# Kernel tuning notes

Hardware: AMD Instinct MI355X
Metric: run time of the kernel (lower is better)

Reference implementation:

```python
import jax, jax.numpy as jnp
import numpy as np

B, N = 2048, 16384
K = 256
TEMPERATURE = 1.0


def entmax15(z):
    # alpha=1.5 entmax via exact sort-based threshold (Peters et al. 2019).
    z = z / 2.0
    zs = jnp.flip(jnp.sort(z, axis=-1), axis=-1)          # descending sort [B, N]
    rho = jnp.arange(1, z.shape[-1] + 1, dtype=z.dtype)   # 1..N
    mean = jnp.cumsum(zs, axis=-1) / rho
    mean_sq = jnp.cumsum(zs * zs, axis=-1) / rho
    ss = rho * (mean_sq - mean * mean)
    delta = jnp.clip((1.0 - ss) / rho, 0.0)
    tau = mean - jnp.sqrt(delta)                           # candidate thresholds
    support = jnp.sum(tau <= zs, axis=-1, keepdims=True)   # support size per row
    tau_star = jnp.take_along_axis(tau, support - 1, axis=-1)
    p = jnp.clip(z - tau_star, 0.0) ** 2
    return p


def setup_inputs() -> dict:
    key = jax.random.key(0)
    logits = jax.random.normal(key, (B, N), dtype=jnp.float32)
    return {"logits": logits}


def reference(logits):
    weights = entmax15(logits / TEMPERATURE)
    # top-k mask + renormalize
    _, topk_idx = jax.lax.top_k(weights, K)                # [B, K]
    mask = jnp.zeros_like(weights).at[
        jnp.arange(weights.shape[0])[:, None], topk_idx
    ].set(1.0)
    weights = weights * mask
    weights = weights / (jnp.sum(weights, axis=-1, keepdims=True) + 1e-8)
    num_selected = jnp.sum(weights > 1e-6, axis=-1)
    return weights, num_selected
```

## Files before the change

kernel.cpp:

```cpp
#include <hip/hip_runtime.h>
#include <math.h>

#define BROWS 2048
#define NCOLS 16384
#define NT    1024
#define V4PT  (NCOLS / NT / 4)
#define CAP   512

__global__ __launch_bounds__(NT, 8)
void entmax_fused(const float* __restrict__ in, float* __restrict__ outw,
                  float* __restrict__ outn)
{
    __shared__ float red[4][16];
    __shared__ float redm[16];
    __shared__ float cand[CAP + 4];
    __shared__ float s_zm, s_T, s_tau, s_S;
    __shared__ int   s_cnt, s_nsel;

    const int row  = blockIdx.x;
    const int tid  = threadIdx.x;
    const int lane = tid & 63;
    const int wid  = tid >> 6;
    const float4* rp4 = (const float4*)(in + (size_t)row * NCOLS);
    float4*       wp4 = (float4*)(outw + (size_t)row * NCOLS);

    if (tid == 0) { s_cnt = 0; s_nsel = 0; }

    float4 zr[V4PT];
    float m = -INFINITY;
    #pragma unroll
    for (int it = 0; it < V4PT; ++it) {
        float4 v = rp4[it * NT + tid];
        v.x *= 0.5f; v.y *= 0.5f; v.z *= 0.5f; v.w *= 0.5f;
        zr[it] = v;
        m = fmaxf(m, fmaxf(fmaxf(v.x, v.y), fmaxf(v.z, v.w)));
    }
    #pragma unroll
    for (int off = 1; off < 64; off <<= 1) m = fmaxf(m, __shfl_xor(m, off));
    if (lane == 0) redm[wid] = m;
    __syncthreads();
    if (tid < 64) {
        float v = (lane < 16) ? redm[lane] : -INFINITY;
        #pragma unroll
        for (int off = 1; off < 16; off <<= 1) v = fmaxf(v, __shfl_xor(v, off));
        if (lane == 0) s_zm = v;
    }
    __syncthreads();
    const float zm = s_zm;

    float g0 = 0.f, g1 = 0.f, g2 = 0.f, g3 = 0.f;
    #pragma unroll
    for (int it = 0; it < V4PT; ++it) {
        float4 v = zr[it];
        #pragma unroll
        for (int e = 0; e < 4; ++e) {
            float z = (e == 0) ? v.x : (e == 1) ? v.y : (e == 2) ? v.z : v.w;
            float d3 = z - (zm - 1.0f);
            if (d3 > 0.f) {
                g3 = fmaf(d3, d3, g3);
                float d2 = d3 - 0.25f; if (d2 > 0.f) g2 = fmaf(d2, d2, g2);
                float d1 = d3 - 0.50f; if (d1 > 0.f) g1 = fmaf(d1, d1, g1);
                float d0 = d3 - 0.75f; if (d0 > 0.f) g0 = fmaf(d0, d0, g0);
            }
        }
    }
    #pragma unroll
    for (int off = 1; off < 64; off <<= 1) {
        g0 += __shfl_xor(g0, off); g1 += __shfl_xor(g1, off);
        g2 += __shfl_xor(g2, off); g3 += __shfl_xor(g3, off);
    }
    if (lane == 0) { red[0][wid] = g0; red[1][wid] = g1; red[2][wid] = g2; red[3][wid] = g3; }
    __syncthreads();
    if (tid < 64) {
        int j = lane >> 4, idx = lane & 15;
        float v = red[j][idx];
        #pragma unroll
        for (int off = 1; off < 16; off <<= 1) v += __shfl_xor(v, off);
        float G0 = __shfl(v, 0), G1 = __shfl(v, 16), G2 = __shfl(v, 32), G3 = __shfl(v, 48);
        (void)G3;
        if (lane == 0) {
            float T = zm - 1.0f;
            if      (G0 >= 1.02f) T = zm - 0.25f;
            else if (G1 >= 1.02f) T = zm - 0.50f;
            else if (G2 >= 1.02f) T = zm - 0.75f;
            s_T = T;
        }
    }
    __syncthreads();
    const float T = s_T;

    #pragma unroll
    for (int it = 0; it < V4PT; ++it) {
        float4 v = zr[it];
        if (v.x > T) { int p = atomicAdd(&s_cnt, 1); if (p < CAP) cand[p] = v.x; }
        if (v.y > T) { int p = atomicAdd(&s_cnt, 1); if (p < CAP) cand[p] = v.y; }
        if (v.z > T) { int p = atomicAdd(&s_cnt, 1); if (p < CAP) cand[p] = v.z; }
        if (v.w > T) { int p = atomicAdd(&s_cnt, 1); if (p < CAP) cand[p] = v.w; }
    }
    __syncthreads();

    if (tid < 64) {
        const int C = min(s_cnt, CAP);
        if (lane < 4) cand[C + lane] = -INFINITY;
        const int C4 = (C + 3) >> 2;
        const float4* c4 = (const float4*)cand;
        float lo = T, hi = zm;
        for (int round = 0; round < 3; ++round) {
            float h = (hi - lo) * 0.015625f;
            float t = fmaf(h, (float)(lane + 1), lo);
            float g = 0.f;
            for (int i = 0; i < C4; ++i) {
                float4 v = c4[i]; float d;
                d = v.x - t; if (d > 0.f) g = fmaf(d, d, g);
                d = v.y - t; if (d > 0.f) g = fmaf(d, d, g);
                d = v.z - t; if (d > 0.f) g = fmaf(d, d, g);
                d = v.w - t; if (d > 0.f) g = fmaf(d, d, g);
            }
            unsigned long long bal = __ballot(g >= 1.f);
            float lo_old = lo;
            if (bal == 0ull) hi = lo_old + h;
            else {
                int j = 63 - (int)__clzll((long long)bal);
                lo = fmaf(h, (float)(j + 1), lo_old);
                hi = fmaf(h, (float)(j + 2), lo_old);
            }
        }
        float tau = lo;
        for (int r = 0; r < 3; ++r) {
            float k = 0.f, s1 = 0.f, s2 = 0.f;
            for (int i = 0; i < C4; ++i) {
                float4 v = c4[i];
                if (v.x > tau) { k += 1.f; s1 += v.x; s2 = fmaf(v.x, v.x, s2); }
                if (v.y > tau) { k += 1.f; s1 += v.y; s2 = fmaf(v.y, v.y, s2); }
                if (v.z > tau) { k += 1.f; s1 += v.z; s2 = fmaf(v.z, v.z, s2); }
                if (v.w > tau) { k += 1.f; s1 += v.w; s2 = fmaf(v.w, v.w, s2); }
            }
            if (k < 0.5f) break;
            float mean  = s1 / k;
            float ss    = s2 - mean * s1;
            float delta = fmaxf((1.f - ss) / k, 0.f);
            tau = mean - sqrtf(delta);
        }
        float ps = 0.f;
        for (int i = 0; i < C4; ++i) {
            float4 v = c4[i]; float d;
            d = v.x - tau; if (d > 0.f) ps = fmaf(d, d, ps);
            d = v.y - tau; if (d > 0.f) ps = fmaf(d, d, ps);
            d = v.z - tau; if (d > 0.f) ps = fmaf(d, d, ps);
            d = v.w - tau; if (d > 0.f) ps = fmaf(d, d, ps);
        }
        if (lane == 0) { s_tau = tau; s_S = ps; }
    }
    __syncthreads();
    const float tau_star = s_tau;
    const float rnorm    = 1.0f / (s_S + 1e-8f);

    int lc = 0;
    #pragma unroll
    for (int it = 0; it < V4PT; ++it) {
        float4 v = zr[it];
        float4 w; float d;
        d = fmaxf(v.x - tau_star, 0.f); w.x = d * d * rnorm; lc += (w.x > 1e-6f);
        d = fmaxf(v.y - tau_star, 0.f); w.y = d * d * rnorm; lc += (w.y > 1e-6f);
        d = fmaxf(v.z - tau_star, 0.f); w.z = d * d * rnorm; lc += (w.z > 1e-6f);
        d = fmaxf(v.w - tau_star, 0.f); w.w = d * d * rnorm; lc += (w.w > 1e-6f);
        wp4[it * NT + tid] = w;
    }
    #pragma unroll
    for (int off = 32; off; off >>= 1) lc += __shfl_down(lc, off);
    if (lane == 0) atomicAdd(&s_nsel, lc);
    __syncthreads();
    if (tid == 0) outn[row] = (float)s_nsel;
}

extern "C" void kernel_launch(void* const* d_in, const int* in_sizes, int n_in,
                              void* d_out, int out_size, void* d_ws, size_t ws_size,
                              hipStream_t stream) {
    const float* logits = (const float*)d_in[0];
    float* outw = (float*)d_out;
    float* outn = outw + (size_t)BROWS * NCOLS;
    entmax_fused<<<dim3(BROWS), dim3(NT), 0, stream>>>(logits, outw, outn);
}
```

Measured before the change: 255.0 us.

## Parallelize candidate threshold search across all warps and use nontemporal stores

The single-warp bisection and Newton-style refinement over the candidate buffer is split across all 16 wavefronts. Partial sums go through shared-memory double buffers, and each thread now redundantly reduces the per-warp partials instead of waiting on an extra barrier-and-broadcast step. This is meant to remove the serial tail where 15 of 16 warps sit idle. The candidate cap grows to 1024 so one candidate maps to one thread, and output stores become nontemporal to avoid polluting the cache. The cost is more barriers and redundant reads of the shared-memory reductions.

```diff
diff --git a/kernel.cpp b/kernel.cpp
--- a/kernel.cpp
+++ b/kernel.cpp
@@ -5,24 +5,28 @@
 #define NCOLS 16384
 #define NT    1024
 #define V4PT  (NCOLS / NT / 4)
-#define CAP   512
+#define NW    (NT / 64)
+#define CAP   1024
+
+typedef float vfloat4 __attribute__((ext_vector_type(4)));
 
 __global__ __launch_bounds__(NT, 8)
 void entmax_fused(const float* __restrict__ in, float* __restrict__ outw,
                   float* __restrict__ outn)
 {
-    __shared__ float red[4][16];
-    __shared__ float redm[16];
-    __shared__ float cand[CAP + 4];
-    __shared__ float s_zm, s_T, s_tau, s_S;
-    __shared__ int   s_cnt, s_nsel;
+    __shared__ float  cand[CAP + 4];
+    __shared__ float  redm[NW];
+    __shared__ float  red[4][NW];
+    __shared__ float  gpart[2][NW][64];
+    __shared__ float4 rpart[2][NW];
+    __shared__ int    s_cnt, s_nsel;
 
-    const int row  = blockIdx.x;
     const int tid  = threadIdx.x;
     const int lane = tid & 63;
     const int wid  = tid >> 6;
+    const int row  = blockIdx.x;
     const float4* rp4 = (const float4*)(in + (size_t)row * NCOLS);
-    float4*       wp4 = (float4*)(outw + (size_t)row * NCOLS);
+    vfloat4*      wp4 = (vfloat4*)(outw + (size_t)row * NCOLS);
 
     if (tid == 0) { s_cnt = 0; s_nsel = 0; }
 
@@ -39,14 +43,9 @@
     for (int off = 1; off < 64; off <<= 1) m = fmaxf(m, __shfl_xor(m, off));
     if (lane == 0) redm[wid] = m;
     __syncthreads();
-    if (tid < 64) {
-        float v = (lane < 16) ? redm[lane] : -INFINITY;
-        #pragma unroll
-        for (int off = 1; off < 16; off <<= 1) v = fmaxf(v, __shfl_xor(v, off));
-        if (lane == 0) s_zm = v;
-    }
-    __syncthreads();
-    const float zm = s_zm;
+    float zm = -INFINITY;
+    #pragma unroll
+    for (int w = 0; w < NW; ++w) zm = fmaxf(zm, redm[w]);
 
     float g0 = 0.f, g1 = 0.f, g2 = 0.f, g3 = 0.f;
     #pragma unroll
@@ -71,23 +70,13 @@
     }
     if (lane == 0) { red[0][wid] = g0; red[1][wid] = g1; red[2][wid] = g2; red[3][wid] = g3; }
     __syncthreads();
-    if (tid < 64) {
-        int j = lane >> 4, idx = lane & 15;
-        float v = red[j][idx];
-        #pragma unroll
-        for (int off = 1; off < 16; off <<= 1) v += __shfl_xor(v, off);
-        float G0 = __shfl(v, 0), G1 = __shfl(v, 16), G2 = __shfl(v, 32), G3 = __shfl(v, 48);
-        (void)G3;
-        if (lane == 0) {
-            float T = zm - 1.0f;
-            if      (G0 >= 1.02f) T = zm - 0.25f;
-            else if (G1 >= 1.02f) T = zm - 0.50f;
-            else if (G2 >= 1.02f) T = zm - 0.75f;
-            s_T = T;
-        }
-    }
-    __syncthreads();
-    const float T = s_T;
+    float G0 = 0.f, G1 = 0.f, G2 = 0.f;
+    #pragma unroll
+    for (int w = 0; w < NW; ++w) { G0 += red[0][w]; G1 += red[1][w]; G2 += red[2][w]; }
+    float T = zm - 1.0f;
+    if      (G0 >= 1.02f) T = zm - 0.25f;
+    else if (G1 >= 1.02f) T = zm - 0.50f;
+    else if (G2 >= 1.02f) T = zm - 0.75f;
 
     #pragma unroll
     for (int it = 0; it < V4PT; ++it) {
@@ -98,73 +87,96 @@
         if (v.w > T) { int p = atomicAdd(&s_cnt, 1); if (p < CAP) cand[p] = v.w; }
     }
     __syncthreads();
+    const int C = min(s_cnt, CAP);
+    if (tid < 4) cand[C + tid] = -INFINITY;
+    __syncthreads();
 
-    if (tid < 64) {
-        const int C = min(s_cnt, CAP);
-        if (lane < 4) cand[C + lane] = -INFINITY;
-        const int C4 = (C + 3) >> 2;
-        const float4* c4 = (const float4*)cand;
-        float lo = T, hi = zm;
-        for (int round = 0; round < 3; ++round) {
-            float h = (hi - lo) * 0.015625f;
-            float t = fmaf(h, (float)(lane + 1), lo);
-            float g = 0.f;
-            for (int i = 0; i < C4; ++i) {
-                float4 v = c4[i]; float d;
-                d = v.x - t; if (d > 0.f) g = fmaf(d, d, g);
-                d = v.y - t; if (d > 0.f) g = fmaf(d, d, g);
-                d = v.z - t; if (d > 0.f) g = fmaf(d, d, g);
-                d = v.w - t; if (d > 0.f) g = fmaf(d, d, g);
-            }
-            unsigned long long bal = __ballot(g >= 1.f);
-            float lo_old = lo;
-            if (bal == 0ull) hi = lo_old + h;
-            else {
-                int j = 63 - (int)__clzll((long long)bal);
-                lo = fmaf(h, (float)(j + 1), lo_old);
-                hi = fmaf(h, (float)(j + 2), lo_old);
-            }
+    const int C4    = (C + 3) >> 2;
+    const int chunk = (C4 + NW - 1) / NW;
+    const int i0    = wid * chunk;
+    const int i1    = min(i0 + chunk, C4);
+    const float4* c4 = (const float4*)cand;
+
+    float lo = T, hi = zm;
+    for (int round = 0; round < 3; ++round) {
+        const int buf = round & 1;
+        float h = (hi - lo) * 0.015625f;
+        float t = fmaf(h, (float)(lane + 1), lo);
+        float g = 0.f;
+        for (int i = i0; i < i1; ++i) {
+            float4 v = c4[i]; float d;
+            d = v.x - t; if (d > 0.f) g = fmaf(d, d, g);
+            d = v.y - t; if (d > 0.f) g = fmaf(d, d, g);
+            d = v.z - t; if (d > 0.f) g = fmaf(d, d, g);
+            d = v.w - t; if (d > 0.f) g = fmaf(d, d, g);
         }
-        float tau = lo;
-        for (int r = 0; r < 3; ++r) {
-            float k = 0.f, s1 = 0.f, s2 = 0.f;
-            for (int i = 0; i < C4; ++i) {
-                float4 v = c4[i];
-                if (v.x > tau) { k += 1.f; s1 += v.x; s2 = fmaf(v.x, v.x, s2); }
-                if (v.y > tau) { k += 1.f; s1 += v.y; s2 = fmaf(v.y, v.y, s2); }
-                if (v.z > tau) { k += 1.f; s1 += v.z; s2 = fmaf(v.z, v.z, s2); }
-                if (v.w > tau) { k += 1.f; s1 += v.w; s2 = fmaf(v.w, v.w, s2); }
-            }
-            if (k < 0.5f) break;
+        gpart[buf][wid][lane] = g;
+        __syncthreads();
+        float gs = 0.f;
+        #pragma unroll
+        for (int w = 0; w < NW; ++w) gs += gpart[buf][w][lane];
+        unsigned long long bal = __ballot(gs >= 1.0f);
+        float lo_old = lo;
+        if (bal == 0ull) hi = lo_old + h;
+        else {
+            int j = 63 - (int)__clzll((long long)bal);
+            lo = fmaf(h, (float)(j + 1), lo_old);
+            hi = fmaf(h, (float)(j + 2), lo_old);
+        }
+    }
+
+    float tau = lo;
+    const float cz = (tid < C) ? cand[tid] : -INFINITY;
+    for (int r = 0; r < 3; ++r) {
+        const int buf = r & 1;
+        float k = 0.f, s1 = 0.f, s2 = 0.f;
+        if (cz > tau) { k = 1.f; s1 = cz; s2 = cz * cz; }
+        #pragma unroll
+        for (int off = 1; off < 64; off <<= 1) {
+            k  += __shfl_xor(k,  off);
+            s1 += __shfl_xor(s1, off);
+            s2 += __shfl_xor(s2, off);
+        }
+        if (lane == 0) rpart[buf][wid] = make_float4(k, s1, s2, 0.f);
+        __syncthreads();
+        k = 0.f; s1 = 0.f; s2 = 0.f;
+        #pragma unroll
+        for (int w = 0; w < NW; ++w) {
+            float4 p = rpart[buf][w]; k += p.x; s1 += p.y; s2 += p.z;
+        }
+        if (k >= 0.5f) {
             float mean  = s1 / k;
             float ss    = s2 - mean * s1;
             float delta = fmaxf((1.f - ss) / k, 0.f);
             tau = mean - sqrtf(delta);
         }
+    }
+
+    float rnorm;
+    {
         float ps = 0.f;
-        for (int i = 0; i < C4; ++i) {
-            float4 v = c4[i]; float d;
-            d = v.x - tau; if (d > 0.f) ps = fmaf(d, d, ps);
-            d = v.y - tau; if (d > 0.f) ps = fmaf(d, d, ps);
-            d = v.z - tau; if (d > 0.f) ps = fmaf(d, d, ps);
-            d = v.w - tau; if (d > 0.f) ps = fmaf(d, d, ps);
-        }
-        if (lane == 0) { s_tau = tau; s_S = ps; }
+        float d = cz - tau;
+        if (d > 0.f) ps = d * d;
+        #pragma unroll
+        for (int off = 1; off < 64; off <<= 1) ps += __shfl_xor(ps, off);
+        if (lane == 0) rpart[1][wid] = make_float4(ps, 0.f, 0.f, 0.f);
+        __syncthreads();
+        float S = 0.f;
+        #pragma unroll
+        for (int w = 0; w < NW; ++w) S += rpart[1][w].x;
+        rnorm = 1.0f / (S + 1e-8f);
     }
-    __syncthreads();
-    const float tau_star = s_tau;
-    const float rnorm    = 1.0f / (s_S + 1e-8f);
 
     int lc = 0;
     #pragma unroll
     for (int it = 0; it < V4PT; ++it) {
         float4 v = zr[it];
-        float4 w; float d;
-        d = fmaxf(v.x - tau_star, 0.f); w.x = d * d * rnorm; lc += (w.x > 1e-6f);
-        d = fmaxf(v.y - tau_star, 0.f); w.y = d * d * rnorm; lc += (w.y > 1e-6f);
-        d = fmaxf(v.z - tau_star, 0.f); w.z = d * d * rnorm; lc += (w.z > 1e-6f);
-        d = fmaxf(v.w - tau_star, 0.f); w.w = d * d * rnorm; lc += (w.w > 1e-6f);
-        wp4[it * NT + tid] = w;
+        vfloat4 w; float d;
+        d = fmaxf(v.x - tau, 0.f); w.x = d * d * rnorm; lc += (w.x > 1e-6f);
+        d = fmaxf(v.y - tau, 0.f); w.y = d * d * rnorm; lc += (w.y > 1e-6f);
+        d = fmaxf(v.z - tau, 0.f); w.z = d * d * rnorm; lc += (w.z > 1e-6f);
+        d = fmaxf(v.w - tau, 0.f); w.w = d * d * rnorm; lc += (w.w > 1e-6f);
+        __builtin_nontemporal_store(w, &wp4[it * NT + tid]);
     }
     #pragma unroll
     for (int off = 32; off; off >>= 1) lc += __shfl_down(lc, off);
```

After: 248.8 us. 1.02x faster.
